# Kernel optimization log

Measured on AMD Instinct MI355X. Metric: run time of the kernel, lower is better.

Reference implementation:

```python
import jax, jax.numpy as jnp
import numpy as np

LN_EPS = 1e-3   # keras LayerNormalization default epsilon
EPS = 1e-5      # module's self.eps
QB = 128.0      # 2**(bits-1) with bits=8


def ste_round(x):
    # straight-through round: forward = round(x), backward = identity
    return x + jax.lax.stop_gradient(jnp.round(x) - x)


def setup_inputs() -> dict:
    key = jax.random.key(0)
    k1, k2 = jax.random.split(key)
    x = jax.random.normal(k1, (4, 8192, 1024), dtype=jnp.float32)
    weight = jax.random.normal(k2, (1024, 1024), dtype=jnp.float32) * 0.02
    ln_gamma = jnp.ones((1024,), dtype=jnp.float32)
    ln_beta = jnp.zeros((1024,), dtype=jnp.float32)
    return {"x": x, "weight": weight, "ln_gamma": ln_gamma, "ln_beta": ln_beta}


def reference(x, weight, ln_gamma, ln_beta):
    # LayerNorm over last axis (keras defaults: eps=1e-3, learnable scale/center)
    mu = jnp.mean(x, axis=-1, keepdims=True)
    var = jnp.var(x, axis=-1, keepdims=True)
    xn = (x - mu) * jax.lax.rsqrt(var + LN_EPS) * ln_gamma + ln_beta

    # 1.58-bit weight ternarization with STE round
    beta = jnp.mean(jnp.abs(weight))                     # per-tensor scale
    w_q = jnp.clip(ste_round(weight / (beta + EPS)), -1.0, 1.0)

    # activation quantization (flg_before_linear=True branch)
    gamma = jnp.max(jnp.abs(xn))                         # per-tensor absmax
    xq = jnp.clip(xn * QB / gamma, -QB + EPS, QB - EPS)

    # quantized matmul + fused rescale
    y = jnp.einsum('bsd,du->bsu', xq, w_q)
    return y * (gamma * beta / QB)
```

## Files before the change

### kernel.cpp

```cpp
#include <hip/hip_runtime.h>
#include <stdint.h>


#define M_ROWS 32768
#define KDIM 1024
#define NDIM 1024

typedef int v4i  __attribute__((ext_vector_type(4)));
typedef int v16i __attribute__((ext_vector_type(16)));

__global__ __launch_bounds__(256) void absum_k(const float* __restrict__ w,
                                               float* __restrict__ partials) {
    int idx = blockIdx.x * 256 + threadIdx.x;
    float4 v = ((const float4*)w)[idx];
    float s = fabsf(v.x) + fabsf(v.y) + fabsf(v.z) + fabsf(v.w);
    #pragma unroll
    for (int o = 32; o; o >>= 1) s += __shfl_xor(s, o);
    __shared__ float p[4];
    if ((threadIdx.x & 63) == 0) p[threadIdx.x >> 6] = s;
    __syncthreads();
    if (threadIdx.x == 0) partials[blockIdx.x] = p[0] + p[1] + p[2] + p[3];
}

__global__ __launch_bounds__(256) void quant_k(const float* __restrict__ w,
                                               const float* __restrict__ partials,
                                               char* __restrict__ wqP,
                                               float* __restrict__ wsum) {
    int t = threadIdx.x;
    float s = partials[t] + partials[t + 256] + partials[t + 512] + partials[t + 768];
    #pragma unroll
    for (int o = 32; o; o >>= 1) s += __shfl_xor(s, o);
    __shared__ float ps[4];
    if ((t & 63) == 0) ps[t >> 6] = s;
    __syncthreads();
    float total = ps[0] + ps[1] + ps[2] + ps[3];
    if (blockIdx.x == 0 && t == 0) wsum[0] = total;
    float beta = total * (1.0f / 1048576.0f);
    float inv  = 1.0f / (beta + 1e-5f);

    __shared__ char sT[64 * 80];
    int k0 = (blockIdx.x >> 4) * 64, n0 = (blockIdx.x & 15) * 64;
    int n_l = t & 63;
    #pragma unroll
    for (int r = 0; r < 16; ++r) {
        int k_l = (t >> 6) * 16 + r;
        float q = rintf(w[(size_t)(k0 + k_l) * NDIM + n0 + n_l] * inv);
        q = fminf(1.0f, fmaxf(-1.0f, q));
        sT[n_l * 80 + k_l] = (char)(int)q;
    }
    __syncthreads();
    int nn = t >> 2, c = t & 3;
    v4i val = *(const v4i*)&sT[nn * 80 + c * 16];
    int n = n0 + nn, k = k0 + c * 16;
    int idx = ((n >> 5) * 32 + (k >> 5)) * 64 + (n & 31) + ((k >> 4) & 1) * 32;
    *(v4i*)&wqP[(size_t)idx * 16] = val;
}

__global__ __launch_bounds__(512, 4) void ln_gemm_k(const float* __restrict__ x,
                                                    const float* __restrict__ g,
                                                    const float* __restrict__ bln,
                                                    const char* __restrict__ wqP,
                                                    const float* __restrict__ wsum,
                                                    float* __restrict__ out) {
    __shared__ char  sA[64 * 1024];
    __shared__ float sScl[64];

    int t = threadIdx.x;
    int w = t >> 6, lane = t & 63;
    int half = lane >> 5, l31 = lane & 31;
    int bm0 = blockIdx.x * 64;

    const v4i* wp = (const v4i*)wqP;
    size_t fb = (size_t)w * 2048 + lane;
    v4i b0 = wp[fb], b1 = wp[fb + 64], b2 = wp[fb + 128], b3 = wp[fb + 192];

    #pragma unroll 1
    for (int rr = 0; rr < 8; ++rr) {
        int row = w * 8 + rr;
        const float4* xr = (const float4*)(x + ((size_t)(bm0 + row) << 10));
        float4 v0 = xr[lane], v1 = xr[lane + 64], v2 = xr[lane + 128], v3 = xr[lane + 192];
        float s  = v0.x + v0.y + v0.z + v0.w + v1.x + v1.y + v1.z + v1.w
                 + v2.x + v2.y + v2.z + v2.w + v3.x + v3.y + v3.z + v3.w;
        float ss = v0.x*v0.x + v0.y*v0.y + v0.z*v0.z + v0.w*v0.w
                 + v1.x*v1.x + v1.y*v1.y + v1.z*v1.z + v1.w*v1.w
                 + v2.x*v2.x + v2.y*v2.y + v2.z*v2.z + v2.w*v2.w
                 + v3.x*v3.x + v3.y*v3.y + v3.z*v3.z + v3.w*v3.w;
        #pragma unroll
        for (int o = 32; o; o >>= 1) { s += __shfl_xor(s, o); ss += __shfl_xor(ss, o); }
        float mu  = s * (1.0f / 1024.0f);
        float var = ss * (1.0f / 1024.0f) - mu * mu;
        float rs  = rsqrtf(var + 1e-3f);
        float xn[16];
        float4 vv[4] = {v0, v1, v2, v3};
        float mx = 0.f;
        #pragma unroll
        for (int j = 0; j < 4; ++j) {
            float4 gg = ((const float4*)g)[lane + 64 * j];
            float4 bb = ((const float4*)bln)[lane + 64 * j];
            xn[4*j+0] = (vv[j].x - mu) * rs * gg.x + bb.x;
            xn[4*j+1] = (vv[j].y - mu) * rs * gg.y + bb.y;
            xn[4*j+2] = (vv[j].z - mu) * rs * gg.z + bb.z;
            xn[4*j+3] = (vv[j].w - mu) * rs * gg.w + bb.w;
            #pragma unroll
            for (int e = 0; e < 4; ++e) mx = fmaxf(mx, fabsf(xn[4*j+e]));
        }
        #pragma unroll
        for (int o = 32; o; o >>= 1) mx = fmaxf(mx, __shfl_xor(mx, o));
        mx = fmaxf(mx, 1e-20f);
        float inv = 127.0f / mx;
        if (lane == 0) sScl[row] = mx * (1.0f / 127.0f);
        int mf = row >> 5, r31 = row & 31;
        #pragma unroll
        for (int j = 0; j < 4; ++j) {
            char4 c4;
            c4.x = (char)(int)rintf(xn[4*j+0] * inv);
            c4.y = (char)(int)rintf(xn[4*j+1] * inv);
            c4.z = (char)(int)rintf(xn[4*j+2] * inv);
            c4.w = (char)(int)rintf(xn[4*j+3] * inv);
            int u    = (lane >> 2) + 16 * j;
            int slot = r31 ^ (u & 7);
            *(char4*)&sA[mf * 32768 + (u * 32 + slot) * 16 + (lane & 3) * 4] = c4;
        }
    }
    __syncthreads();

    float beta = wsum[0] * (1.0f / 1048576.0f);

    #define LA(dst, S) do { \
        int u_ = 2 * (S) + half; \
        int o_ = ((u_ * 32) + (l31 ^ (u_ & 7))) * 16; \
        dst[0] = *(const v4i*)&sA[o_]; \
        dst[1] = *(const v4i*)&sA[o_ + 32768]; \
    } while (0)
    #define BSEL(q_) wp[fb + (size_t)((q_) & 31) * 64 + ((((q_) >= 32) && (p < 3)) ? 16384u : 0u)]

    v4i aA[2], aB[2];
    LA(aA, 0); LA(aB, 1);

    #pragma unroll 1
    for (int p = 0; p < 4; ++p) {
        v16i acc0 = {}, acc1 = {};
        #pragma unroll 1
        for (int s = 0; s < 32; s += 4) {
            acc0 = __builtin_amdgcn_mfma_i32_32x32x32_i8(aA[0], b0, acc0, 0, 0, 0);
            acc1 = __builtin_amdgcn_mfma_i32_32x32x32_i8(aA[1], b0, acc1, 0, 0, 0);
            b0 = BSEL(s + 4);
            LA(aA, s + 2);
            acc0 = __builtin_amdgcn_mfma_i32_32x32x32_i8(aB[0], b1, acc0, 0, 0, 0);
            acc1 = __builtin_amdgcn_mfma_i32_32x32x32_i8(aB[1], b1, acc1, 0, 0, 0);
            b1 = BSEL(s + 5);
            LA(aB, s + 3);
            acc0 = __builtin_amdgcn_mfma_i32_32x32x32_i8(aA[0], b2, acc0, 0, 0, 0);
            acc1 = __builtin_amdgcn_mfma_i32_32x32x32_i8(aA[1], b2, acc1, 0, 0, 0);
            b2 = BSEL(s + 6);
            LA(aA, (s + 4) & 31);
            acc0 = __builtin_amdgcn_mfma_i32_32x32x32_i8(aB[0], b3, acc0, 0, 0, 0);
            acc1 = __builtin_amdgcn_mfma_i32_32x32x32_i8(aB[1], b3, acc1, 0, 0, 0);
            b3 = BSEL(s + 7);
            LA(aB, (s + 5) & 31);
        }

        int nb = p * 8 + w;
        #pragma unroll
        for (int r = 0; r < 16; ++r) {
            int rl = (r & 3) + 8 * (r >> 2) + 4 * half;
            float sc0 = sScl[rl] * beta;
            float sc1 = sScl[32 + rl] * beta;
            size_t o = (size_t)(bm0 + rl) * NDIM + nb * 32 + l31;
            out[o]                     = (float)acc0[r] * sc0;
            out[o + (size_t)32 * NDIM] = (float)acc1[r] * sc1;
        }
        fb += 16384;
    }
    #undef LA
    #undef BSEL
}

extern "C" void kernel_launch(void* const* d_in, const int* in_sizes, int n_in,
                              void* d_out, int out_size, void* d_ws, size_t ws_size,
                              hipStream_t stream) {
    const float* x        = (const float*)d_in[0];
    const float* weight   = (const float*)d_in[1];
    const float* ln_gamma = (const float*)d_in[2];
    const float* ln_beta  = (const float*)d_in[3];
    float* out = (float*)d_out;

    float* wsum     = (float*)d_ws;
    float* partials = (float*)((char*)d_ws + 4096);
    char*  wqP      = (char*)d_ws + (1u << 18);

    absum_k<<<1024, 256, 0, stream>>>(weight, partials);
    quant_k<<<256, 256, 0, stream>>>(weight, partials, wqP, wsum);
    ln_gemm_k<<<M_ROWS / 64, 512, 0, stream>>>(x, ln_gamma, ln_beta, wqP, wsum, out);
}
```

Baseline: 283.1 us.

## Widen per-wave GEMM tile to 64x64 with four accumulators, fully unrolled

```diff
diff --git a/kernel.cpp b/kernel.cpp
--- a/kernel.cpp
+++ b/kernel.cpp
@@ -8,6 +8,8 @@
 
 typedef int v4i  __attribute__((ext_vector_type(4)));
 typedef int v16i __attribute__((ext_vector_type(16)));
+
+#define MFMA_I8 __builtin_amdgcn_mfma_i32_32x32x32_i8
 
 __global__ __launch_bounds__(256) void absum_k(const float* __restrict__ w,
                                                float* __restrict__ partials) {
@@ -71,8 +73,9 @@
     int bm0 = blockIdx.x * 64;
 
     const v4i* wp = (const v4i*)wqP;
-    size_t fb = (size_t)w * 2048 + lane;
-    v4i b0 = wp[fb], b1 = wp[fb + 64], b2 = wp[fb + 128], b3 = wp[fb + 192];
+    size_t fb = (size_t)w * 4096 + lane;
+    v4i bX0 = wp[fb],        bX1 = wp[fb + 2048];
+    v4i bY0 = wp[fb + 64],   bY1 = wp[fb + 2048 + 64];
 
     #pragma unroll 1
     for (int rr = 0; rr < 8; ++rr) {
@@ -126,54 +129,58 @@
 
     float beta = wsum[0] * (1.0f / 1048576.0f);
 
-    #define LA(dst, S) do { \
+    #define LA2(dst, S) do { \
         int u_ = 2 * (S) + half; \
         int o_ = ((u_ * 32) + (l31 ^ (u_ & 7))) * 16; \
         dst[0] = *(const v4i*)&sA[o_]; \
         dst[1] = *(const v4i*)&sA[o_ + 32768]; \
     } while (0)
-    #define BSEL(q_) wp[fb + (size_t)((q_) & 31) * 64 + ((((q_) >= 32) && (p < 3)) ? 16384u : 0u)]
-
-    v4i aA[2], aB[2];
-    LA(aA, 0); LA(aB, 1);
 
     #pragma unroll 1
-    for (int p = 0; p < 4; ++p) {
-        v16i acc0 = {}, acc1 = {};
-        #pragma unroll 1
-        for (int s = 0; s < 32; s += 4) {
-            acc0 = __builtin_amdgcn_mfma_i32_32x32x32_i8(aA[0], b0, acc0, 0, 0, 0);
-            acc1 = __builtin_amdgcn_mfma_i32_32x32x32_i8(aA[1], b0, acc1, 0, 0, 0);
-            b0 = BSEL(s + 4);
-            LA(aA, s + 2);
-            acc0 = __builtin_amdgcn_mfma_i32_32x32x32_i8(aB[0], b1, acc0, 0, 0, 0);
-            acc1 = __builtin_amdgcn_mfma_i32_32x32x32_i8(aB[1], b1, acc1, 0, 0, 0);
-            b1 = BSEL(s + 5);
-            LA(aB, s + 3);
-            acc0 = __builtin_amdgcn_mfma_i32_32x32x32_i8(aA[0], b2, acc0, 0, 0, 0);
-            acc1 = __builtin_amdgcn_mfma_i32_32x32x32_i8(aA[1], b2, acc1, 0, 0, 0);
-            b2 = BSEL(s + 6);
-            LA(aA, (s + 4) & 31);
-            acc0 = __builtin_amdgcn_mfma_i32_32x32x32_i8(aB[0], b3, acc0, 0, 0, 0);
-            acc1 = __builtin_amdgcn_mfma_i32_32x32x32_i8(aB[1], b3, acc1, 0, 0, 0);
-            b3 = BSEL(s + 7);
-            LA(aB, (s + 5) & 31);
-        }
-
-        int nb = p * 8 + w;
+    for (int p = 0; p < 2; ++p) {
+        v16i a00 = {}, a01 = {}, a10 = {}, a11 = {};
+        v4i aX[2], aY[2];
+        LA2(aX, 0); LA2(aY, 1);
+
+        #pragma unroll
+        for (int s = 0; s < 32; s += 2) {
+            a00 = MFMA_I8(aX[0], bX0, a00, 0, 0, 0);
+            a10 = MFMA_I8(aX[1], bX0, a10, 0, 0, 0);
+            if (s < 30) bX0 = wp[fb + (size_t)(s + 2) * 64];
+            a01 = MFMA_I8(aX[0], bX1, a01, 0, 0, 0);
+            a11 = MFMA_I8(aX[1], bX1, a11, 0, 0, 0);
+            if (s < 30) bX1 = wp[fb + 2048 + (size_t)(s + 2) * 64];
+            if (s < 30) LA2(aX, s + 2);
+            a00 = MFMA_I8(aY[0], bY0, a00, 0, 0, 0);
+            a10 = MFMA_I8(aY[1], bY0, a10, 0, 0, 0);
+            if (s < 30) bY0 = wp[fb + (size_t)(s + 3) * 64];
+            a01 = MFMA_I8(aY[0], bY1, a01, 0, 0, 0);
+            a11 = MFMA_I8(aY[1], bY1, a11, 0, 0, 0);
+            if (s < 30) bY1 = wp[fb + 2048 + (size_t)(s + 3) * 64];
+            if (s < 30) LA2(aY, s + 3);
+        }
+
+        if (p == 0) {
+            fb += 32768;
+            bX0 = wp[fb];      bX1 = wp[fb + 2048];
+            bY0 = wp[fb + 64]; bY1 = wp[fb + 2048 + 64];
+        }
+
+        int nb0 = p * 16 + w * 2;
         #pragma unroll
         for (int r = 0; r < 16; ++r) {
             int rl = (r & 3) + 8 * (r >> 2) + 4 * half;
             float sc0 = sScl[rl] * beta;
             float sc1 = sScl[32 + rl] * beta;
-            size_t o = (size_t)(bm0 + rl) * NDIM + nb * 32 + l31;
-            out[o]                     = (float)acc0[r] * sc0;
-            out[o + (size_t)32 * NDIM] = (float)acc1[r] * sc1;
-        }
-        fb += 16384;
+            size_t o0 = (size_t)(bm0 + rl) * NDIM + nb0 * 32 + l31;
+            size_t o1 = o0 + (size_t)32 * NDIM;
+            out[o0]      = (float)a00[r] * sc0;
+            out[o0 + 32] = (float)a01[r] * sc0;
+            out[o1]      = (float)a10[r] * sc1;
+            out[o1 + 32] = (float)a11[r] * sc1;
+        }
     }
-    #undef LA
-    #undef BSEL
+    #undef LA2
 }
 
 extern "C" void kernel_launch(void* const* d_in, const int* in_sizes, int n_in,
```

After: 449.0 us. 1.59x slower.
